# Performance work log

Measured on AMD Instinct MI355X. Metric: run time of the kernel, lower is better.

The kernel has to match this reference:

```python
import jax, jax.numpy as jnp
import numpy as np

V, H = 30522, 768          # vocab, hidden (bert-base)
B, S, E = 32, 512, 8       # batch, seq_len, entities per example
KG_DIM, MLP_HID = 100, 1000


def setup_inputs() -> dict:
    key = jax.random.key(0)
    k0, k1, k2, k3, k4 = jax.random.split(key, 5)
    input_ids = jax.random.randint(k0, (B, S), 0, V)
    entity_embeddings = jax.random.normal(k1, (B, E, KG_DIM), dtype=jnp.float32)
    # binary span mask: each entity covers a few token positions
    entity_mask = (jax.random.uniform(k2, (B, E, S)) < 0.02).astype(jnp.float32)
    word_embedding = jax.random.normal(k3, (V, H), dtype=jnp.float32) * 0.02
    k5, k6 = jax.random.split(k4)
    W1 = jax.random.normal(k5, (KG_DIM, MLP_HID), dtype=jnp.float32) * 0.02
    b1 = jnp.zeros((MLP_HID,), dtype=jnp.float32)
    W2 = jax.random.normal(k6, (MLP_HID, H), dtype=jnp.float32) * 0.02
    b2 = jnp.zeros((H,), dtype=jnp.float32)
    return {"input_ids": input_ids, "entity_embeddings": entity_embeddings,
            "entity_mask": entity_mask, "word_embedding": word_embedding,
            "W1": W1, "b1": b1, "W2": W2, "b2": b2}


def reference(input_ids, entity_embeddings, entity_mask, word_embedding, W1, b1, W2, b2):
    # gather token embeddings: [B,S,H]
    inputs_embeds = word_embedding[input_ids]
    # tiny MLP on entity (KG) embeddings: [B,E,100] -> [B,E,H]
    h = jax.nn.relu(jnp.einsum('bek,kh->beh', entity_embeddings, W1) + b1)
    ent = jnp.einsum('beh,hd->bed', h, W2) + b2
    # masked scatter-add of entity vectors into token positions
    # (batched form of entity_mask[S,1].mm(entity_emb[1,H]) accumulated over entities)
    inputs_embeds = inputs_embeds + jnp.einsum('bes,beh->bsh', entity_mask, ent)
    return inputs_embeds
```

## Files before the change

### kernel.cpp

```cpp
#include <hip/hip_runtime.h>

#define VV   30522
#define HH   768
#define BB   32
#define SS   512
#define EE   8
#define KGD  100
#define MHID 1000

#define RTOT (BB * EE)
#define KS   5
#define KC   (MHID / KS)

__global__ __launch_bounds__(256) void mlp1_kernel(
    const float* __restrict__ ee,
    const float* __restrict__ W1,
    const float* __restrict__ b1,
    const float* __restrict__ b2,
    float* __restrict__ h,
    float* __restrict__ ent)
{
    __shared__ float sEE[KGD];
    const int r   = blockIdx.x;
    const int tid = threadIdx.x;

    for (int i = tid; i < KGD; i += 256)
        sEE[i] = ee[r * KGD + i];

    for (int i = tid; i < HH; i += 256)
        ent[r * HH + i] = b2[i];
    __syncthreads();

    const int j0 = tid;
    const int j1 = tid + 256;
    const int j2 = tid + 512;
    const int j3v = tid + 768;
    const bool v3 = (j3v < MHID);
    const int j3 = v3 ? j3v : (MHID - 1);

    float a0 = b1[j0], a1 = b1[j1], a2 = b1[j2], a3 = b1[j3];
    #pragma unroll 2
    for (int k = 0; k < KGD; ++k) {
        const float x = sEE[k];
        const float* w = &W1[k * MHID];
        a0 = fmaf(x, w[j0], a0);
        a1 = fmaf(x, w[j1], a1);
        a2 = fmaf(x, w[j2], a2);
        a3 = fmaf(x, w[j3], a3);
    }
    float* hr = &h[r * MHID];
    hr[j0] = fmaxf(a0, 0.0f);
    hr[j1] = fmaxf(a1, 0.0f);
    hr[j2] = fmaxf(a2, 0.0f);
    if (v3) hr[j3] = fmaxf(a3, 0.0f);
}

__global__ __launch_bounds__(256) void mlp2_kernel(
    const float* __restrict__ h,
    const float* __restrict__ W2,
    float* __restrict__ ent)
{
    __shared__ float sH[EE * KC];

    const int dt = blockIdx.x / KS;
    const int kc = blockIdx.x % KS;
    const int b  = blockIdx.y;
    const int tid = threadIdx.x;

    for (int i = tid; i < EE * KC; i += 256) {
        const int e = i / KC;
        const int j = i - e * KC;
        sH[i] = h[(b * EE + e) * MHID + kc * KC + j];
    }
    __syncthreads();

    const int c  = tid & 63;
    const int g  = tid >> 6;
    const int e0 = 2 * g;
    const int d  = dt * 64 + c;

    float acc0 = 0.0f, acc1 = 0.0f;
    const float* h0 = &sH[e0 * KC];
    const float* h1 = &sH[(e0 + 1) * KC];
    const float* w  = &W2[(size_t)(kc * KC) * HH + d];
    #pragma unroll 4
    for (int j = 0; j < KC; ++j) {
        const float wv = w[(size_t)j * HH];
        acc0 = fmaf(h0[j], wv, acc0);
        acc1 = fmaf(h1[j], wv, acc1);
    }
    atomicAdd(&ent[(b * EE + e0) * HH + d], acc0);
    atomicAdd(&ent[(b * EE + e0 + 1) * HH + d], acc1);
}

__global__ __launch_bounds__(256) void gather_scatter_kernel(
    const int*   __restrict__ ids,
    const float* __restrict__ mask,
    const float* __restrict__ we,
    const float* __restrict__ ent,
    float* __restrict__ out)
{
    const int row = blockIdx.x * 4 + (threadIdx.x >> 6);
    const int l   = threadIdx.x & 63;
    const int b   = row >> 9;
    const int s   = row & (SS - 1);

    const int id = ids[row];
    const float4* wrow = reinterpret_cast<const float4*>(we + (size_t)id * HH);
    float4 v0 = wrow[l];
    float4 v1 = wrow[l + 64];
    float4 v2 = wrow[l + 128];

    const float* mrow = mask + (size_t)b * EE * SS + s;
    #pragma unroll
    for (int e = 0; e < EE; ++e) {
        const float m = mrow[e * SS];
        if (m != 0.0f) {
            const float4* er =
                reinterpret_cast<const float4*>(ent + (size_t)(b * EE + e) * HH);
            const float4 e0 = er[l], e1 = er[l + 64], e2 = er[l + 128];
            v0.x = fmaf(m, e0.x, v0.x); v0.y = fmaf(m, e0.y, v0.y);
            v0.z = fmaf(m, e0.z, v0.z); v0.w = fmaf(m, e0.w, v0.w);
            v1.x = fmaf(m, e1.x, v1.x); v1.y = fmaf(m, e1.y, v1.y);
            v1.z = fmaf(m, e1.z, v1.z); v1.w = fmaf(m, e1.w, v1.w);
            v2.x = fmaf(m, e2.x, v2.x); v2.y = fmaf(m, e2.y, v2.y);
            v2.z = fmaf(m, e2.z, v2.z); v2.w = fmaf(m, e2.w, v2.w);
        }
    }
    float4* orow = reinterpret_cast<float4*>(out + (size_t)row * HH);
    orow[l]       = v0;
    orow[l + 64]  = v1;
    orow[l + 128] = v2;
}

extern "C" void kernel_launch(void* const* d_in, const int* in_sizes, int n_in,
                              void* d_out, int out_size, void* d_ws, size_t ws_size,
                              hipStream_t stream) {
    const int*   input_ids = (const int*)  d_in[0];
    const float* ent_emb   = (const float*)d_in[1];
    const float* ent_mask  = (const float*)d_in[2];
    const float* word_emb  = (const float*)d_in[3];
    const float* W1        = (const float*)d_in[4];
    const float* b1        = (const float*)d_in[5];
    const float* W2        = (const float*)d_in[6];
    const float* b2        = (const float*)d_in[7];
    float*       out       = (float*)d_out;

    float* ent = (float*)d_ws;
    float* h   = (float*)d_ws + (size_t)RTOT * HH;

    mlp1_kernel<<<dim3(RTOT), dim3(256), 0, stream>>>(
        ent_emb, W1, b1, b2, h, ent);

    mlp2_kernel<<<dim3(12 * KS, BB), dim3(256), 0, stream>>>(
        h, W2, ent);

    gather_scatter_kernel<<<dim3(BB * SS / 4), dim3(256), 0, stream>>>(
        input_ids, ent_mask, word_emb, ent, out);
}
```

Before: 220.7 us.

## Split MLP1 across two blocks, deepen MLP2 K-split, use nontemporal output stores

The first MLP kernel now splits its 1000 hidden outputs across two blocks per row, doubling the grid so more blocks run at once. The second MLP uses 8 K-chunks instead of 5, giving more blocks and more atomics. KC becomes 125, so the unroll factor changes to 5. The gather/scatter kernel switches to ext_vector float4 arithmetic and writes its output with nontemporal stores, so the large output stream bypasses cache retention. The bulk of the time is the memory-bound gather and write of 50MB, so gains depend mainly on the nontemporal stores.

```diff
diff --git a/kernel.cpp b/kernel.cpp
--- a/kernel.cpp
+++ b/kernel.cpp
@@ -9,8 +9,10 @@
 #define MHID 1000
 
 #define RTOT (BB * EE)
-#define KS   5
+#define KS   8
 #define KC   (MHID / KS)
+
+typedef float f32x4 __attribute__((ext_vector_type(4)));
 
 __global__ __launch_bounds__(256) void mlp1_kernel(
     const float* __restrict__ ee,
@@ -22,37 +24,35 @@
 {
     __shared__ float sEE[KGD];
     const int r   = blockIdx.x;
+    const int jc  = blockIdx.y;
     const int tid = threadIdx.x;
 
-    for (int i = tid; i < KGD; i += 256)
-        sEE[i] = ee[r * KGD + i];
+    if (tid < KGD) sEE[tid] = ee[r * KGD + tid];
 
-    for (int i = tid; i < HH; i += 256)
-        ent[r * HH + i] = b2[i];
+    {
+        const int base = jc * (HH / 2);
+        for (int i = tid; i < HH / 2; i += 256)
+            ent[r * HH + base + i] = b2[base + i];
+    }
     __syncthreads();
 
-    const int j0 = tid;
-    const int j1 = tid + 256;
-    const int j2 = tid + 512;
-    const int j3v = tid + 768;
-    const bool v3 = (j3v < MHID);
-    const int j3 = v3 ? j3v : (MHID - 1);
+    const int j0  = jc * 512 + tid;
+    const int j1v = jc * 512 + tid + 256;
+    const bool v1 = (j1v < MHID);
+    const int j1  = v1 ? j1v : (MHID - 1);
 
-    float a0 = b1[j0], a1 = b1[j1], a2 = b1[j2], a3 = b1[j3];
-    #pragma unroll 2
+    float a0 = b1[j0];
+    float a1 = b1[j1];
+    #pragma unroll 4
     for (int k = 0; k < KGD; ++k) {
         const float x = sEE[k];
         const float* w = &W1[k * MHID];
         a0 = fmaf(x, w[j0], a0);
         a1 = fmaf(x, w[j1], a1);
-        a2 = fmaf(x, w[j2], a2);
-        a3 = fmaf(x, w[j3], a3);
     }
     float* hr = &h[r * MHID];
     hr[j0] = fmaxf(a0, 0.0f);
-    hr[j1] = fmaxf(a1, 0.0f);
-    hr[j2] = fmaxf(a2, 0.0f);
-    if (v3) hr[j3] = fmaxf(a3, 0.0f);
+    if (v1) hr[j1] = fmaxf(a1, 0.0f);
 }
 
 __global__ __launch_bounds__(256) void mlp2_kernel(
@@ -83,7 +83,7 @@
     const float* h0 = &sH[e0 * KC];
     const float* h1 = &sH[(e0 + 1) * KC];
     const float* w  = &W2[(size_t)(kc * KC) * HH + d];
-    #pragma unroll 4
+    #pragma unroll 5
     for (int j = 0; j < KC; ++j) {
         const float wv = w[(size_t)j * HH];
         acc0 = fmaf(h0[j], wv, acc0);
@@ -106,31 +106,28 @@
     const int s   = row & (SS - 1);
 
     const int id = ids[row];
-    const float4* wrow = reinterpret_cast<const float4*>(we + (size_t)id * HH);
-    float4 v0 = wrow[l];
-    float4 v1 = wrow[l + 64];
-    float4 v2 = wrow[l + 128];
+    const f32x4* wrow = reinterpret_cast<const f32x4*>(we + (size_t)id * HH);
+    f32x4 v0 = wrow[l];
+    f32x4 v1 = wrow[l + 64];
+    f32x4 v2 = wrow[l + 128];
 
     const float* mrow = mask + (size_t)b * EE * SS + s;
     #pragma unroll
     for (int e = 0; e < EE; ++e) {
         const float m = mrow[e * SS];
         if (m != 0.0f) {
-            const float4* er =
-                reinterpret_cast<const float4*>(ent + (size_t)(b * EE + e) * HH);
-            const float4 e0 = er[l], e1 = er[l + 64], e2 = er[l + 128];
-            v0.x = fmaf(m, e0.x, v0.x); v0.y = fmaf(m, e0.y, v0.y);
-            v0.z = fmaf(m, e0.z, v0.z); v0.w = fmaf(m, e0.w, v0.w);
-            v1.x = fmaf(m, e1.x, v1.x); v1.y = fmaf(m, e1.y, v1.y);
-            v1.z = fmaf(m, e1.z, v1.z); v1.w = fmaf(m, e1.w, v1.w);
-            v2.x = fmaf(m, e2.x, v2.x); v2.y = fmaf(m, e2.y, v2.y);
-            v2.z = fmaf(m, e2.z, v2.z); v2.w = fmaf(m, e2.w, v2.w);
+            const f32x4* er =
+                reinterpret_cast<const f32x4*>(ent + (size_t)(b * EE + e) * HH);
+            const f32x4 e0 = er[l], e1 = er[l + 64], e2 = er[l + 128];
+            v0 += m * e0;
+            v1 += m * e1;
+            v2 += m * e2;
         }
     }
-    float4* orow = reinterpret_cast<float4*>(out + (size_t)row * HH);
-    orow[l]       = v0;
-    orow[l + 64]  = v1;
-    orow[l + 128] = v2;
+    f32x4* orow = reinterpret_cast<f32x4*>(out + (size_t)row * HH);
+    __builtin_nontemporal_store(v0, &orow[l]);
+    __builtin_nontemporal_store(v1, &orow[l + 64]);
+    __builtin_nontemporal_store(v2, &orow[l + 128]);
 }
 
 extern "C" void kernel_launch(void* const* d_in, const int* in_sizes, int n_in,
@@ -149,7 +146,7 @@
     float* ent = (float*)d_ws;
     float* h   = (float*)d_ws + (size_t)RTOT * HH;
 
-    mlp1_kernel<<<dim3(RTOT), dim3(256), 0, stream>>>(
+    mlp1_kernel<<<dim3(RTOT, 2), dim3(256), 0, stream>>>(
         ent_emb, W1, b1, b2, h, ent);
 
     mlp2_kernel<<<dim3(12 * KS, BB), dim3(256), 0, stream>>>(
```

Result: faster. 207.5 us (-6.0%).
